# Optimization experiments

Hardware: AMD Instinct MI355X
Metric: run time of the kernel (lower is better)

## Reference

```python
import jax, jax.numpy as jnp
import numpy as np
from jax import lax

H = W = 200          # feature map size
STRIDE = 16
IMG_H = IMG_W = H * STRIDE  # 3200
C = 512
A = 9                # 3 scales x 3 aspect ratios
K_PRE = 1000         # pre-NMS topk (hardcoded in module)
K_POST = 100         # post-NMS keep (hardcoded in module)
IOU_TH = 0.7


def make_anchors():
    scales = jnp.array([128.0, 256.0, 512.0], dtype=jnp.float32)
    ratios = jnp.array([0.5, 1.0, 2.0], dtype=jnp.float32)
    hr = jnp.sqrt(ratios)                      # (3,)
    wr = 1.0 / hr
    ws = (wr[:, None] * scales[None, :]).reshape(-1)   # (9,)
    hs = (hr[:, None] * scales[None, :]).reshape(-1)
    base = jnp.stack([-ws / 2, -hs / 2, ws / 2, hs / 2], axis=1)  # (9,4)
    sx = jnp.arange(W, dtype=jnp.float32) * STRIDE
    sy = jnp.arange(H, dtype=jnp.float32) * STRIDE
    gy, gx = jnp.meshgrid(sy, sx, indexing='ij')
    shifts = jnp.stack([gx, gy, gx, gy], axis=-1).reshape(-1, 4)  # (H*W,4)
    return (shifts[:, None, :] + base[None, :, :]).reshape(-1, 4)  # (H*W*A,4)


def decode(anchors, deltas):
    w = anchors[:, 2] - anchors[:, 0]
    h = anchors[:, 3] - anchors[:, 1]
    cx = anchors[:, 0] + 0.5 * w
    cy = anchors[:, 1] + 0.5 * h
    px = deltas[:, 0] * w + cx
    py = deltas[:, 1] * h + cy
    pw = jnp.exp(deltas[:, 2]) * w
    ph = jnp.exp(deltas[:, 3]) * h
    return jnp.stack([px - 0.5 * pw, py - 0.5 * ph, px + 0.5 * pw, py + 0.5 * ph], axis=1)


def clamp_boxes(b):
    return jnp.stack([
        jnp.clip(b[:, 0], 0.0, IMG_W), jnp.clip(b[:, 1], 0.0, IMG_H),
        jnp.clip(b[:, 2], 0.0, IMG_W), jnp.clip(b[:, 3], 0.0, IMG_H)], axis=1)


def nms_keep(boxes, thr):
    # boxes (K_PRE,4) already sorted by descending score (topk output order)
    x1, y1, x2, y2 = boxes[:, 0], boxes[:, 1], boxes[:, 2], boxes[:, 3]
    areas = (x2 - x1) * (y2 - y1)
    idx = jnp.arange(K_PRE)

    def body(i, keep):
        iw = jnp.clip(jnp.minimum(x2[i], x2) - jnp.maximum(x1[i], x1), 0.0)
        ih = jnp.clip(jnp.minimum(y2[i], y2) - jnp.maximum(y1[i], y1), 0.0)
        inter = iw * ih
        iou = inter / (areas[i] + areas - inter)
        supp = (iou > thr) & (idx > i) & keep[i]
        return keep & jnp.logical_not(supp)

    return lax.fori_loop(0, K_PRE, body, jnp.ones(K_PRE, dtype=bool))


def rpn_forward(feat, conv_w, conv_b, cls_w, cls_b, reg_w, reg_b):
    dn = ('NCHW', 'OIHW', 'NCHW')
    x = lax.conv_general_dilated(feat, conv_w, (1, 1), 'SAME', dimension_numbers=dn)
    x = jax.nn.relu(x + conv_b[None, :, None, None])
    cls = lax.conv_general_dilated(x, cls_w, (1, 1), 'SAME', dimension_numbers=dn) + cls_b[None, :, None, None]
    reg = lax.conv_general_dilated(x, reg_w, (1, 1), 'SAME', dimension_numbers=dn) + reg_b[None, :, None, None]
    # (1,A,H,W) -> (H*W*A,)
    cls_logits = cls.transpose(0, 2, 3, 1).reshape(-1)
    # (1,A*4,H,W) -> (H*W*A,4)
    deltas = reg.reshape(1, A, 4, H, W).transpose(0, 3, 4, 1, 2).reshape(-1, 4)
    anchors = make_anchors()
    proposals = decode(anchors, deltas)
    scores = jax.nn.sigmoid(cls_logits)
    top_sc, top_idx = lax.top_k(scores, K_PRE)           # sorted descending
    props = clamp_boxes(proposals[top_idx])
    keep = lax.stop_gradient(nms_keep(props, IOU_TH))    # NMS decision is non-diff
    # kept indices, in score order (stable sort puts kept first, preserving order)
    order = jnp.argsort(jnp.where(keep, 0, 1), stable=True)[:K_POST]
    valid = jnp.arange(K_POST) < jnp.sum(keep)
    out_boxes = jnp.where(valid[:, None], props[order], 0.0)
    out_scores = jnp.where(valid, top_sc[order], 0.0)
    return out_boxes, out_scores


def setup_inputs() -> dict:
    key = jax.random.key(0)
    ks = jax.random.split(key, 7)
    s = 0.02
    return {
        'feat': jax.random.normal(ks[0], (1, C, H, W), dtype=jnp.float32),
        'conv_w': jax.random.normal(ks[1], (C, C, 3, 3), dtype=jnp.float32) * s,
        'conv_b': jnp.zeros((C,), dtype=jnp.float32),
        'cls_w': jax.random.normal(ks[2], (A, C, 1, 1), dtype=jnp.float32) * s,
        'cls_b': jnp.zeros((A,), dtype=jnp.float32),
        'reg_w': jax.random.normal(ks[3], (A * 4, C, 1, 1), dtype=jnp.float32) * s,
        'reg_b': jnp.zeros((A * 4,), dtype=jnp.float32),
    }


def reference(feat, conv_w, conv_b, cls_w, cls_b, reg_w, reg_b):
    return rpn_forward(feat, conv_w, conv_b, cls_w, cls_b, reg_w, reg_b)
```

## Files before the change

### kernel.cpp

```cpp
#include <hip/hip_runtime.h>
#include <stdint.h>

static constexpr int H_ = 200, W_ = 200, HW_ = 40000;
static constexpr int C_ = 512;
static constexpr int NANCH = 360000;
static constexpr int KPRE = 1000;
static constexpr int KPOST = 100;
static constexpr int KSEL = 1400;
static constexpr int PXCAP = 4096;
static constexpr int KSPLIT = 8;
static constexpr int FT = 212;
static constexpr int FP = 202;

typedef __attribute__((ext_vector_type(8))) short bf16x8;
typedef __attribute__((ext_vector_type(4))) float f32x4;

__device__ inline ushort f2bf(float f) {
    unsigned u = __float_as_uint(f);
    u += 0x7FFFu + ((u >> 16) & 1u);
    return (ushort)(u >> 16);
}
__device__ inline float bf2f(ushort h) { return __uint_as_float(((unsigned)h) << 16); }

typedef const __attribute__((address_space(1))) uint32_t gas_u32;
typedef __attribute__((address_space(3))) uint32_t las_u32;
__device__ __forceinline__ void gload_lds16(const void* g, void* l) {
    __builtin_amdgcn_global_load_lds((gas_u32*)(uintptr_t)g, (las_u32*)(uintptr_t)l, 16, 0, 0);
}

__global__ void k_zero_u32(unsigned* __restrict__ p, int n) {
    int i = blockIdx.x * 256 + threadIdx.x;
    if (i < n) p[i] = 0u;
}

__global__ void k_zero_border_t(ushort* __restrict__ feat_t) {
    int t = blockIdx.x * 256 + threadIdx.x;
    int total = 4944 * 64;
    if (t >= total) return;
    int px = t >> 6, part = t & 63;
    int y, x;
    if (px < 2544) { int ri = px / 212; x = px - ri * 212; y = (ri == 0) ? 0 : 200 + ri; }
    else { int q = px - 2544; int r12 = q / 12; int c = q - r12 * 12; y = 1 + r12; x = (c == 0) ? 0 : 200 + c; }
    uint4 z = {0u, 0u, 0u, 0u};
    *(uint4*)&feat_t[((size_t)y * FT + x) * 512 + part * 8] = z;
}

__global__ void k_zero_border_px(float* __restrict__ feat_px) {
    int t = blockIdx.x * 256 + threadIdx.x;
    int total = 804 * 128;
    if (t >= total) return;
    int px = t >> 7, part = t & 127;
    int y, x;
    if (px < 202)      { y = 0;   x = px; }
    else if (px < 404) { y = 201; x = px - 202; }
    else if (px < 604) { x = 0;   y = 1 + (px - 404); }
    else               { x = 201; y = 1 + (px - 604); }
    float4 z = {0.f, 0.f, 0.f, 0.f};
    *(float4*)&feat_px[((size_t)y * FP + x) * 512 + part * 4] = z;
}

__global__ void k_feat_t(const float* __restrict__ feat, ushort* __restrict__ feat_t) {
    __shared__ ushort lt[32 * 8 * 33];
    int x0 = blockIdx.x * 32, y0 = blockIdx.y * 8, ci0 = blockIdx.z * 32;
    int tid = threadIdx.x;
    for (int u = tid; u < 8192; u += 256) {
        int ciL = u >> 8, rem = u & 255;
        int yy = rem >> 5, xx = rem & 31;
        int x = x0 + xx;
        float v = (x < W_) ? feat[(size_t)(ci0 + ciL) * HW_ + (y0 + yy) * W_ + x] : 0.f;
        lt[(ciL * 8 + yy) * 33 + xx] = f2bf(v);
    }
    __syncthreads();
    for (int u = tid; u < 1024; u += 256) {
        int pxu = u >> 2, part = u & 3;
        int yy = pxu >> 5, xx = pxu & 31;
        if (x0 + xx >= W_) continue;
        ushort tmp[8];
#pragma unroll
        for (int k = 0; k < 8; ++k) tmp[k] = lt[((part * 8 + k) * 8 + yy) * 33 + xx];
        *(uint4*)&feat_t[((size_t)(y0 + yy + 1) * FT + (x0 + xx + 1)) * 512 + ci0 + part * 8] =
            *(const uint4*)&tmp[0];
    }
}

__global__ void k_feat_px(const float* __restrict__ feat, float* __restrict__ feat_px) {
    __shared__ float lt[32 * 8 * 33];
    int x0 = blockIdx.x * 32, y0 = blockIdx.y * 8, ci0 = blockIdx.z * 32;
    int tid = threadIdx.x;
    for (int u = tid; u < 8192; u += 256) {
        int ciL = u >> 8, rem = u & 255;
        int yy = rem >> 5, xx = rem & 31;
        int x = x0 + xx;
        float v = (x < W_) ? feat[(size_t)(ci0 + ciL) * HW_ + (y0 + yy) * W_ + x] : 0.f;
        lt[(ciL * 8 + yy) * 33 + xx] = v;
    }
    __syncthreads();
    for (int u = tid; u < 1024; u += 256) {
        int pxu = u >> 2, part = u & 3;
        int yy = pxu >> 5, xx = pxu & 31;
        if (x0 + xx >= W_) continue;
        float tmp[8];
#pragma unroll
        for (int k = 0; k < 8; ++k) tmp[k] = lt[((part * 8 + k) * 8 + yy) * 33 + xx];
        float* dst = &feat_px[((size_t)(y0 + yy + 1) * FP + (x0 + xx + 1)) * 512 + ci0 + part * 8];
        *(float4*)&dst[0] = *(const float4*)&tmp[0];
        *(float4*)&dst[4] = *(const float4*)&tmp[4];
    }
}

__global__ void k_wt_both(const float* __restrict__ conv_w, ushort* __restrict__ wt_t,
                          float* __restrict__ wt_ex) {
    __shared__ float t[32][33];
    int kb = blockIdx.x * 32;
    int cb = blockIdx.y * 32;
    int lx = threadIdx.x, ly = threadIdx.y;
    int tap = kb >> 9, ci0 = kb & 511;
    for (int r = ly; r < 32; r += 8) {
        float v = conv_w[((size_t)(cb + r) * 512 + ci0 + lx) * 9 + tap];
        t[r][lx] = v;
        wt_t[(size_t)tap * 262144 + (size_t)(cb + r) * 512 + ci0 + lx] = f2bf(v);
    }
    __syncthreads();
    for (int r = ly; r < 32; r += 8)
        wt_ex[(size_t)(kb + r) * 512 + cb + lx] = t[lx][r];
}

__global__ __launch_bounds__(256)
__attribute__((amdgpu_waves_per_eu(2, 4)))
void k_conv3_mfma(const ushort* __restrict__ feat_t, const ushort* __restrict__ wt_t,
                  const float* __restrict__ bias, ushort* __restrict__ xab) {
    __shared__ ushort halo[18 * 34 * 32];
    __shared__ ushort wtile[9 * 64 * 32];
    int b = blockIdx.x;
    int cot = b & 7;
    int tile = b >> 3;
    int xt = tile % 7, yt = tile / 7;
    int x0 = xt * 32, y0 = yt * 16;
    int co0 = cot * 64;
    int tid = threadIdx.x;
    int lane = tid & 63, wid = tid >> 6;
    int l15 = lane & 15, l4 = lane >> 4;

    f32x4 acc[4][2][4];
#pragma unroll
    for (int i = 0; i < 4; ++i)
#pragma unroll
        for (int h = 0; h < 2; ++h)
#pragma unroll
            for (int j = 0; j < 4; ++j) acc[i][h][j] = (f32x4){0.f, 0.f, 0.f, 0.f};

    for (int ch = 0; ch < 16; ++ch) {
        int ci0 = ch * 32;
        __syncthreads();
        for (int u = tid; u < 2448; u += 256) {
            int p = u >> 2, q = u & 3;
            int r = p / 34, c = p - r * 34;
            const ushort* src = feat_t + ((size_t)(y0 + r) * FT + (x0 + c)) * 512 + ci0 + q * 8;
            gload_lds16(src, &halo[(u & ~63) * 8]);
        }
        for (int u = tid; u < 2304; u += 256) {
            int row = u >> 2, q = u & 3;
            int tap = row >> 6, co = row & 63;
            const ushort* src = wt_t + ((size_t)(tap * 512 + co0 + co)) * 512 + ci0 + q * 8;
            gload_lds16(src, &wtile[(u & ~63) * 8]);
        }
        __syncthreads();
#pragma unroll
        for (int tap = 0; tap < 9; ++tap) {
            int th = tap / 3, tw = tap - th * 3;
            bf16x8 af[4][2];
#pragma unroll
            for (int pi = 0; pi < 4; ++pi)
#pragma unroll
                for (int xh = 0; xh < 2; ++xh)
                    af[pi][xh] = *(const bf16x8*)&halo[
                        ((wid * 4 + pi + th) * 34 + (xh * 16 + l15 + tw)) * 32 + l4 * 8];
#pragma unroll
            for (int cj = 0; cj < 4; ++cj) {
                bf16x8 bf = *(const bf16x8*)&wtile[(tap * 64 + cj * 16 + l15) * 32 + l4 * 8];
#pragma unroll
                for (int pi = 0; pi < 4; ++pi)
#pragma unroll
                    for (int xh = 0; xh < 2; ++xh)
                        acc[pi][xh][cj] = __builtin_amdgcn_mfma_f32_16x16x32_bf16(
                            af[pi][xh], bf, acc[pi][xh][cj], 0, 0, 0);
            }
        }
    }

    float bv[4];
#pragma unroll
    for (int cj = 0; cj < 4; ++cj) bv[cj] = bias[co0 + cj * 16 + l15];
#pragma unroll
    for (int pi = 0; pi < 4; ++pi) {
        int yy = y0 + wid * 4 + pi;
        if (yy >= H_) continue;
#pragma unroll
        for (int xh = 0; xh < 2; ++xh) {
#pragma unroll
            for (int cj = 0; cj < 4; ++cj) {
                int co = co0 + cj * 16 + l15;
#pragma unroll
                for (int r = 0; r < 4; ++r) {
                    int xx = x0 + xh * 16 + l4 * 4 + r;
                    if (xx < W_) {
                        float v = acc[pi][xh][cj][r] + bv[cj];
                        xab[((size_t)(yy * W_ + xx)) * 512 + co] = f2bf(v > 0.f ? v : 0.f);
                    }
                }
            }
        }
    }
}

__global__ void k_cls(const ushort* __restrict__ xab, const float* __restrict__ cls_w,
                      const float* __restrict__ cls_b, float* __restrict__ scores) {
    __shared__ ushort xt[64 * 520];
    int t = threadIdx.x;
    int pxb = blockIdx.x * 64;
    for (int i = 0; i < 64; ++i)
        *(uint4*)&xt[i * 520 + t * 8] =
            *(const uint4*)&xab[((size_t)(pxb + i)) * 512 + t * 8];
    __syncthreads();
    float acc[9];
#pragma unroll
    for (int a = 0; a < 9; ++a) acc[a] = 0.f;
    const ushort* row = &xt[t * 520];
    for (int k = 0; k < 64; ++k) {
        bf16x8 v = *(const bf16x8*)&row[k * 8];
        float xv[8];
#pragma unroll
        for (int j = 0; j < 8; ++j) xv[j] = bf2f((ushort)v[j]);
#pragma unroll
        for (int a = 0; a < 9; ++a)
#pragma unroll
            for (int j = 0; j < 8; ++j)
                acc[a] = fmaf(xv[j], cls_w[a * 512 + k * 8 + j], acc[a]);
    }
    int px = pxb + t;
#pragma unroll
    for (int a = 0; a < 9; ++a)
        scores[(size_t)px * 9 + a] = 1.f / (1.f + expf(-(acc[a] + cls_b[a])));
}

__global__ void k_hist1_lds(const float* __restrict__ scores, unsigned* __restrict__ hist) {
    __shared__ unsigned h[16384];
    int tid = threadIdx.x;
    for (int j = tid; j < 16384; j += 256) h[j] = 0u;
    __syncthreads();
    int stride = gridDim.x * 256;
    for (int i = blockIdx.x * 256 + tid; i < NANCH; i += stride)
        atomicAdd(&h[(__float_as_uint(scores[i]) >> 16) & 16383], 1u);
    __syncthreads();
    for (int j = tid; j < 16384; j += 256) {
        unsigned v = h[j];
        if (v) atomicAdd(&hist[j], v);
    }
}

__global__ void k_find_thr(const unsigned* __restrict__ hist, unsigned* __restrict__ meta,
                           int mode, int Kwant) {
    __shared__ unsigned csum[1024];
    int t = threadIdx.x;
    unsigned base = (mode == 0) ? 0u : meta[1];
    unsigned s = 0;
    for (int b = 0; b < 64; ++b) s += hist[t * 64 + b];
    csum[t] = s;
    __syncthreads();
    for (int off = 1; off < 1024; off <<= 1) {
        unsigned add = (t + off < 1024) ? csum[t + off] : 0u;
        __syncthreads();
        csum[t] += add;
        __syncthreads();
    }
    unsigned run = base + ((t < 1023) ? csum[t + 1] : 0u);
    for (int b = 63; b >= 0; --b) {
        unsigned h = hist[t * 64 + b];
        if (run < (unsigned)Kwant && run + h >= (unsigned)Kwant) {
            if (mode == 0) {
                meta[0] = (unsigned)(t * 64 + b);
                meta[1] = run;
            } else {
                meta[2] = (meta[0] << 16) | (unsigned)(t * 64 + b);
                meta[3] = run;
                meta[4] = (unsigned)Kwant - run;
            }
            break;
        }
        run += h;
    }
}

__global__ void k_collect_cand(const float* __restrict__ scores, const unsigned* __restrict__ meta,
                               unsigned* __restrict__ flags) {
    int i = blockIdx.x * 256 + threadIdx.x;
    if (i >= NANCH) return;
    if ((__float_as_uint(scores[i]) >> 16) >= meta[0]) flags[i / 9] = 1u;
}

__global__ void k_px_compact(unsigned* __restrict__ flags, unsigned* __restrict__ meta,
                             unsigned* __restrict__ px_list) {
    int px = blockIdx.x * 256 + threadIdx.x;
    if (px >= HW_) return;
    if (flags[px]) {
        unsigned s = atomicAdd(&meta[10], 1u);
        if (s < (unsigned)PXCAP) { px_list[s] = (unsigned)px; flags[px] = s + 1u; }
        else flags[px] = 0u;
    }
}

__global__ __attribute__((amdgpu_waves_per_eu(2, 4)))
void k_exact_gemm(const float* __restrict__ feat_px, const float* __restrict__ wt_ex,
                  const unsigned* __restrict__ meta, const unsigned* __restrict__ px_list,
                  float* __restrict__ xpart) {
    int npx = (int)meta[10]; if (npx > PXCAP) npx = PXCAP;
    int pb = blockIdx.x;
    if (pb * 64 >= npx) return;
    int cot = blockIdx.y;
    int kz = blockIdx.z;
    __shared__ float A[64][68];
    __shared__ float B[64][68];
    __shared__ int plist[64];
    int tid = threadIdx.x;
    int co0 = cot * 64;
    if (tid < 64) {
        int slot = pb * 64 + tid;
        plist[tid] = (slot < npx) ? (int)px_list[slot] : (int)px_list[0];
    }
    int tcog = tid >> 4;
    int tpxg = tid & 15;
    float acc[4][4];
#pragma unroll
    for (int i = 0; i < 4; ++i)
#pragma unroll
        for (int j = 0; j < 4; ++j) acc[i][j] = 0.f;
    int kbase = kz * 576;
    for (int kc = 0; kc < 9; ++kc) {
        int k0 = kbase + kc * 64;
        __syncthreads();
        for (int u = tid; u < 1024; u += 256) {
            int k = u >> 4, cp = (u & 15) * 4;
            *(float4*)&A[k][cp] = *(const float4*)&wt_ex[(size_t)(k0 + k) * 512 + co0 + cp];
        }
#pragma unroll
        for (int hh = 0; hh < 2; ++hh) {
            int kh = k0 + hh * 32;
            int tap = kh >> 9, ci0c = kh & 511;
            int th = tap / 3, tw = tap - th * 3;
            for (int u = tid; u < 512; u += 256) {
                int s = u >> 3, part = u & 7;
                int px = plist[s];
                int y = px / W_, x = px - y * W_;
                float4 v = *(const float4*)&feat_px[((size_t)(y + th) * FP + (x + tw)) * 512 + ci0c + part * 4];
                B[hh * 32 + part * 4 + 0][s] = v.x; B[hh * 32 + part * 4 + 1][s] = v.y;
                B[hh * 32 + part * 4 + 2][s] = v.z; B[hh * 32 + part * 4 + 3][s] = v.w;
            }
        }
        __syncthreads();
#pragma unroll 4
        for (int k = 0; k < 64; ++k) {
            float wv[4], pv[4];
            *(float4*)&wv[0] = *(const float4*)&A[k][tcog * 4];
            *(float4*)&pv[0] = *(const float4*)&B[k][tpxg * 4];
#pragma unroll
            for (int i = 0; i < 4; ++i)
#pragma unroll
                for (int j = 0; j < 4; ++j) acc[i][j] = fmaf(wv[i], pv[j], acc[i][j]);
        }
    }
#pragma unroll
    for (int j = 0; j < 4; ++j) {
        int slot = pb * 64 + tpxg * 4 + j;
        if (slot >= npx) continue;
        f32x4 tmp;
        tmp[0] = acc[0][j]; tmp[1] = acc[1][j]; tmp[2] = acc[2][j]; tmp[3] = acc[3][j];
        __builtin_nontemporal_store(tmp,
            (f32x4*)&xpart[((size_t)kz * PXCAP + slot) * 512 + co0 + tcog * 4]);
    }
}

__global__ void k_exact_fin(const float* __restrict__ xpart, const float* __restrict__ bias,
                            const float* __restrict__ cls_w, const float* __restrict__ cls_b,
                            const unsigned* __restrict__ meta,
                            float* __restrict__ xex, float* __restrict__ scores_ex) {
    int slot = blockIdx.x;
    int npx = (int)meta[10]; if (npx > PXCAP) npx = PXCAP;
    if (slot >= npx) return;
    int l = threadIdx.x;
    float xv[8];
#pragma unroll
    for (int j = 0; j < 8; ++j) {
        int co = j * 64 + l;
        float v = 0.f;
#pragma unroll
        for (int kz = 0; kz < KSPLIT; ++kz)
            v += __builtin_nontemporal_load(&xpart[((size_t)kz * PXCAP + slot) * 512 + co]);
        v += bias[co];
        v = v > 0.f ? v : 0.f;
        xex[(size_t)slot * 512 + co] = v;
        xv[j] = v;
    }
#pragma unroll
    for (int a = 0; a < 9; ++a) {
        float s = 0.f;
#pragma unroll
        for (int k = 0; k < 8; ++k) s = fmaf(xv[k], cls_w[a * 512 + k * 64 + l], s);
#pragma unroll
        for (int o = 32; o > 0; o >>= 1) s += __shfl_down(s, o);
        if (l == 0) scores_ex[slot * 9 + a] = 1.f / (1.f + expf(-(s + cls_b[a])));
    }
}

__global__ void k_hist1_ex_lds(const float* __restrict__ scores_ex, const unsigned* __restrict__ meta,
                               unsigned* __restrict__ hist) {
    __shared__ unsigned h[16384];
    int npx = (int)meta[10]; if (npx > PXCAP) npx = PXCAP;
    int n = npx * 9;
    int tid = threadIdx.x;
    for (int j = tid; j < 16384; j += 256) h[j] = 0u;
    __syncthreads();
    for (int i = blockIdx.x * 256 + tid; i < n; i += 32 * 256)
        atomicAdd(&h[(__float_as_uint(scores_ex[i]) >> 16) & 16383], 1u);
    __syncthreads();
    for (int j = tid; j < 16384; j += 256) {
        unsigned v = h[j];
        if (v) atomicAdd(&hist[j], v);
    }
}

__global__ void k_hist2_ex(const float* __restrict__ scores_ex, const unsigned* __restrict__ meta,
                           const unsigned* __restrict__ meta_ex, unsigned* __restrict__ hist2) {
    int npx = (int)meta[10]; if (npx > PXCAP) npx = PXCAP;
    int i = blockIdx.x * 256 + threadIdx.x;
    if (i >= npx * 9) return;
    unsigned b = __float_as_uint(scores_ex[i]);
    if ((b >> 16) == meta_ex[0]) atomicAdd(&hist2[b & 0xFFFFu], 1u);
}

__global__ void k_collect_ex(const float* __restrict__ scores_ex, const unsigned* __restrict__ meta,
                             unsigned* __restrict__ meta_ex, const unsigned* __restrict__ px_list,
                             unsigned* __restrict__ sel_bits, unsigned* __restrict__ sel_idx,
                             unsigned* __restrict__ eq_idx) {
    int npx = (int)meta[10]; if (npx > PXCAP) npx = PXCAP;
    int i = blockIdx.x * 256 + threadIdx.x;
    if (i >= npx * 9) return;
    unsigned b = __float_as_uint(scores_ex[i]);
    unsigned T = meta_ex[2];
    unsigned g = px_list[i / 9] * 9u + (unsigned)(i % 9);
    if (b > T) {
        unsigned s = atomicAdd(&meta_ex[8], 1u);
        if (s < 1024u) { sel_bits[s] = b; sel_idx[s] = g; }
    } else if (b == T) {
        unsigned s = atomicAdd(&meta_ex[9], 1u);
        if (s < 65536u) eq_idx[s] = g;
    }
}

__global__ void k_topk_final(const unsigned* __restrict__ sel_bits, const unsigned* __restrict__ sel_idx,
                             const unsigned* __restrict__ eq_idx, const unsigned* __restrict__ meta,
                             unsigned* __restrict__ top_idx, float* __restrict__ top_sc) {
    __shared__ uint64_t keys[1024];
    __shared__ int lcnt;
    __shared__ int lred;
    int t = threadIdx.x;
    unsigned cntGt = meta[3];
    unsigned need = meta[4];
    unsigned cntEq = meta[9];
    unsigned T = meta[2];

    unsigned idx_cut = 0xFFFFFFFFu;
    if (cntEq > need) {
        unsigned lo = 0, hi = NANCH - 1;
        while (lo < hi) {
            unsigned mid = (lo + hi) >> 1;
            int c = 0;
            for (unsigned e = t; e < cntEq; e += 1024)
                if (eq_idx[e] <= mid) c++;
            if (t == 0) lred = 0;
            __syncthreads();
            atomicAdd(&lred, c);
            __syncthreads();
            int tot = lred;
            __syncthreads();
            if ((unsigned)tot >= need) hi = mid; else lo = mid + 1;
        }
        idx_cut = lo;
    }

    keys[t] = 0ull;
    if (t == 0) lcnt = 0;
    __syncthreads();
    for (unsigned s = t; s < cntGt; s += 1024)
        keys[s] = ((uint64_t)sel_bits[s] << 32) | (uint64_t)(0xFFFFFFFFu - sel_idx[s]);
    for (unsigned e = t; e < cntEq; e += 1024) {
        unsigned ix = eq_idx[e];
        if (ix <= idx_cut) {
            int s2 = (int)cntGt + atomicAdd(&lcnt, 1);
            keys[s2] = ((uint64_t)T << 32) | (uint64_t)(0xFFFFFFFFu - ix);
        }
    }
    __syncthreads();
    for (int k = 2; k <= 1024; k <<= 1) {
        for (int j = k >> 1; j > 0; j >>= 1) {
            int ixj = t ^ j;
            if (ixj > t) {
                uint64_t a = keys[t], b = keys[ixj];
                bool desc = (t & k) == 0;
                if (desc ? (a < b) : (a > b)) { keys[t] = b; keys[ixj] = a; }
            }
            __syncthreads();
        }
    }
    if (t < KPRE) {
        top_sc[t] = __uint_as_float((unsigned)(keys[t] >> 32));
        top_idx[t] = 0xFFFFFFFFu - (unsigned)keys[t];
    }
}

__global__ void k_decode(const float* __restrict__ xex, const unsigned* __restrict__ flags,
                         const float* __restrict__ reg_w, const float* __restrict__ reg_b,
                         const unsigned* __restrict__ top_idx,
                         float* __restrict__ props, float* __restrict__ areas) {
    int j = blockIdx.x;
    int lane = threadIdx.x;
    unsigned idx = top_idx[j];
    int pix = (int)(idx / 9u);
    int a = (int)(idx - (unsigned)pix * 9u);
    int slot = (int)flags[pix] - 1;
    if (slot < 0) slot = 0;
    const float* xr = xex + (size_t)slot * 512;
    float s0 = 0, s1 = 0, s2 = 0, s3 = 0;
    for (int c = lane; c < C_; c += 64) {
        float xv = xr[c];
        s0 = fmaf(xv, reg_w[(a * 4 + 0) * C_ + c], s0);
        s1 = fmaf(xv, reg_w[(a * 4 + 1) * C_ + c], s1);
        s2 = fmaf(xv, reg_w[(a * 4 + 2) * C_ + c], s2);
        s3 = fmaf(xv, reg_w[(a * 4 + 3) * C_ + c], s3);
    }
#pragma unroll
    for (int o = 32; o > 0; o >>= 1) {
        s0 += __shfl_down(s0, o);
        s1 += __shfl_down(s1, o);
        s2 += __shfl_down(s2, o);
        s3 += __shfl_down(s3, o);
    }
    if (lane == 0) {
        float d0 = s0 + reg_b[a * 4 + 0];
        float d1 = s1 + reg_b[a * 4 + 1];
        float d2 = s2 + reg_b[a * 4 + 2];
        float d3 = s3 + reg_b[a * 4 + 3];
        int h = pix / W_, w2 = pix - h * W_;
        int rr = a / 3, ss = a - rr * 3;
        float ratio = (rr == 0) ? 0.5f : (rr == 1) ? 1.0f : 2.0f;
        float scale = (ss == 0) ? 128.f : (ss == 1) ? 256.f : 512.f;
        float hr = sqrtf(ratio);
        float wr = 1.0f / hr;
        float wsc = wr * scale, hsc = hr * scale;
        float sx = (float)w2 * 16.f, sy = (float)h * 16.f;
        float a0 = sx - wsc * 0.5f, a1 = sy - hsc * 0.5f;
        float a2 = sx + wsc * 0.5f, a3 = sy + hsc * 0.5f;
        float bw = a2 - a0, bh = a3 - a1;
        float cx = a0 + 0.5f * bw, cy = a1 + 0.5f * bh;
        float px = d0 * bw + cx, py = d1 * bh + cy;
        float pw = expf(d2) * bw, ph = expf(d3) * bh;
        float b0 = px - 0.5f * pw, b1 = py - 0.5f * ph;
        float b2 = px + 0.5f * pw, b3 = py + 0.5f * ph;
        b0 = fminf(fmaxf(b0, 0.f), 3200.f);
        b1 = fminf(fmaxf(b1, 0.f), 3200.f);
        b2 = fminf(fmaxf(b2, 0.f), 3200.f);
        b3 = fminf(fmaxf(b3, 0.f), 3200.f);
        props[j * 4 + 0] = b0;
        props[j * 4 + 1] = b1;
        props[j * 4 + 2] = b2;
        props[j * 4 + 3] = b3;
        areas[j] = (b2 - b0) * (b3 - b1);
    }
}

__global__ void k_nms_mask(const float* __restrict__ props, const float* __restrict__ areas,
                           unsigned long long* __restrict__ mask, float* __restrict__ out) {
    int i = blockIdx.x;
    int tid = threadIdx.x;
    if (i == 0) {
        for (int t = tid; t < KPOST * 5; t += 256) out[t] = 0.f;
    }
    float x1i = props[i * 4 + 0], y1i = props[i * 4 + 1];
    float x2i = props[i * 4 + 2], y2i = props[i * 4 + 3];
    float ai = areas[i];
#pragma unroll
    for (int k = 0; k < 4; ++k) {
        int j = k * 256 + tid;
        bool sup = false;
        if (j < KPRE && j > i) {
            float iw = fminf(x2i, props[j * 4 + 2]) - fmaxf(x1i, props[j * 4 + 0]);
            float ih = fminf(y2i, props[j * 4 + 3]) - fmaxf(y1i, props[j * 4 + 1]);
            iw = fmaxf(iw, 0.f);
            ih = fmaxf(ih, 0.f);
            float inter = iw * ih;
            float iou = inter / (ai + areas[j] - inter);
            sup = iou > 0.7f;
        }
        unsigned long long b = __ballot(sup);
        int word = k * 4 + (tid >> 6);
        if ((tid & 63) == 0) mask[(size_t)i * 16 + word] = b;
    }
}

__global__ void k_nms_scan_out(const unsigned long long* __restrict__ mask,
                               const float* __restrict__ props, const float* __restrict__ top_sc,
                               float* __restrict__ out) {
    __shared__ int kidx[KPOST];
    __shared__ int nk;
    int lane = threadIdx.x;
    if (lane == 0) {
        unsigned long long k0 = ~0ull, k1 = ~0ull, k2 = ~0ull, k3 = ~0ull;
        unsigned long long k4 = ~0ull, k5 = ~0ull, k6 = ~0ull, k7 = ~0ull;
        unsigned long long k8 = ~0ull, k9 = ~0ull, k10 = ~0ull, k11 = ~0ull;
        unsigned long long k12 = ~0ull, k13 = ~0ull, k14 = ~0ull;
        unsigned long long k15 = (1ull << 40) - 1ull;
        int kept = 0;
#define APPLY_ROW(ii) { const unsigned long long* row = &mask[(size_t)(ii) * 16];          \
        k0 &= ~row[0];  k1 &= ~row[1];  k2 &= ~row[2];  k3 &= ~row[3];                     \
        k4 &= ~row[4];  k5 &= ~row[5];  k6 &= ~row[6];  k7 &= ~row[7];                     \
        k8 &= ~row[8];  k9 &= ~row[9];  k10 &= ~row[10]; k11 &= ~row[11];                  \
        k12 &= ~row[12]; k13 &= ~row[13]; k14 &= ~row[14]; k15 &= ~row[15]; }
#define SCAN_WORD(w, kw) { \
        unsigned long long rem = kw; \
        while (rem) { \
            int b = __builtin_ctzll(rem); \
            kidx[kept++] = (w) * 64 + b; \
            if (kept == KPOST) goto done; \
            APPLY_ROW((w) * 64 + b); \
            rem &= kw; \
            rem &= (b >= 63) ? 0ull : ~((2ull << b) - 1ull); \
        } }
        SCAN_WORD(0, k0)  SCAN_WORD(1, k1)  SCAN_WORD(2, k2)  SCAN_WORD(3, k3)
        SCAN_WORD(4, k4)  SCAN_WORD(5, k5)  SCAN_WORD(6, k6)  SCAN_WORD(7, k7)
        SCAN_WORD(8, k8)  SCAN_WORD(9, k9)  SCAN_WORD(10, k10) SCAN_WORD(11, k11)
        SCAN_WORD(12, k12) SCAN_WORD(13, k13) SCAN_WORD(14, k14) SCAN_WORD(15, k15)
done:
        nk = kept;
#undef SCAN_WORD
#undef APPLY_ROW
    }
    __syncthreads();
    int n = nk;
    for (int t = lane; t < KPOST; t += 64) {
        if (t < n) {
            int i = kidx[t];
            out[t * 4 + 0] = props[i * 4 + 0];
            out[t * 4 + 1] = props[i * 4 + 1];
            out[t * 4 + 2] = props[i * 4 + 2];
            out[t * 4 + 3] = props[i * 4 + 3];
            out[KPOST * 4 + t] = top_sc[i];
        }
    }
}

extern "C" void kernel_launch(void* const* d_in, const int* in_sizes, int n_in,
                              void* d_out, int out_size, void* d_ws, size_t ws_size,
                              hipStream_t stream) {
    const float* feat   = (const float*)d_in[0];
    const float* conv_w = (const float*)d_in[1];
    const float* conv_b = (const float*)d_in[2];
    const float* cls_w  = (const float*)d_in[3];
    const float* cls_b  = (const float*)d_in[4];
    const float* reg_w  = (const float*)d_in[5];
    const float* reg_b  = (const float*)d_in[6];
    float* out = (float*)d_out;

    size_t off = 0;
    auto alloc = [&](size_t bytes) -> void* {
        off = (off + 255) & ~(size_t)255;
        void* p = (char*)d_ws + off;
        off += bytes;
        return p;
    };
    ushort* feat_t  = (ushort*)alloc((size_t)FT * FT * 512 * 2);
    float*  feat_px = (float*)alloc((size_t)FP * FP * 512 * 4);
    ushort* wt_t    = (ushort*)alloc((size_t)9 * 512 * 512 * 2);
    float*  wt_ex   = (float*)alloc((size_t)9 * 512 * 512 * 4);
    ushort* xab     = (ushort*)alloc((size_t)HW_ * 512 * 2);
    float*  xpart   = (float*)alloc((size_t)KSPLIT * PXCAP * 512 * 4);
    float*  xex     = (float*)alloc((size_t)PXCAP * 512 * 4);
    float*  scores  = (float*)alloc((size_t)NANCH * 4);
    float*  scores_ex = (float*)alloc((size_t)PXCAP * 9 * 4);
    unsigned* hist1   = (unsigned*)alloc(65536 * 4);
    unsigned* hist2   = (unsigned*)alloc(65536 * 4);
    unsigned* hist1e  = (unsigned*)alloc(65536 * 4);
    unsigned* hist2e  = (unsigned*)alloc(65536 * 4);
    unsigned* meta    = (unsigned*)alloc(64 * 4);
    unsigned* meta_ex = (unsigned*)alloc(64 * 4);
    unsigned* flags   = (unsigned*)alloc((size_t)HW_ * 4);
    unsigned* px_list = (unsigned*)alloc(PXCAP * 4);
    unsigned* sel_bits = (unsigned*)alloc(1024 * 4);
    unsigned* sel_idx  = (unsigned*)alloc(1024 * 4);
    unsigned* eq_idx   = (unsigned*)alloc(65536 * 4);
    unsigned* top_idx  = (unsigned*)alloc(KPRE * 4);
    float* top_sc      = (float*)alloc(KPRE * 4);
    float* props       = (float*)alloc(KPRE * 4 * 4);
    float* areas       = (float*)alloc(KPRE * 4);
    unsigned long long* mask = (unsigned long long*)alloc((size_t)KPRE * 16 * 8);
    (void)ws_size; (void)in_sizes; (void)n_in; (void)out_size;

    k_zero_border_t<<<(4944 * 64 + 255) / 256, 256, 0, stream>>>(feat_t);
    int zrDw = 65536 * 4 + 128 + HW_;
    k_zero_u32<<<(zrDw + 255) / 256, 256, 0, stream>>>(hist1, zrDw);
    k_feat_t<<<dim3(7, 25, 16), 256, 0, stream>>>(feat, feat_t);
    k_wt_both<<<dim3(144, 16), dim3(32, 8), 0, stream>>>(conv_w, wt_t, wt_ex);
    k_conv3_mfma<<<8 * 91, 256, 0, stream>>>(feat_t, wt_t, conv_b, xab);
    k_cls<<<HW_ / 64, 64, 0, stream>>>(xab, cls_w, cls_b, scores);
    k_hist1_lds<<<64, 256, 0, stream>>>(scores, hist1);
    k_find_thr<<<1, 1024, 0, stream>>>(hist1, meta, 0, KSEL);
    k_collect_cand<<<(NANCH + 255) / 256, 256, 0, stream>>>(scores, meta, flags);
    k_px_compact<<<(HW_ + 255) / 256, 256, 0, stream>>>(flags, meta, px_list);
    k_zero_border_px<<<(804 * 128 + 255) / 256, 256, 0, stream>>>(feat_px);
    k_feat_px<<<dim3(7, 25, 16), 256, 0, stream>>>(feat, feat_px);
    k_exact_gemm<<<dim3(PXCAP / 64, 8, KSPLIT), 256, 0, stream>>>(feat_px, wt_ex, meta, px_list, xpart);
    k_exact_fin<<<PXCAP, 64, 0, stream>>>(xpart, conv_b, cls_w, cls_b, meta, xex, scores_ex);
    k_hist1_ex_lds<<<32, 256, 0, stream>>>(scores_ex, meta, hist1e);
    k_find_thr<<<1, 1024, 0, stream>>>(hist1e, meta_ex, 0, KPRE);
    k_hist2_ex<<<(PXCAP * 9 + 255) / 256, 256, 0, stream>>>(scores_ex, meta, meta_ex, hist2e);
    k_find_thr<<<1, 1024, 0, stream>>>(hist2e, meta_ex, 1, KPRE);
    k_collect_ex<<<(PXCAP * 9 + 255) / 256, 256, 0, stream>>>(scores_ex, meta, meta_ex, px_list,
                                                              sel_bits, sel_idx, eq_idx);
    k_topk_final<<<1, 1024, 0, stream>>>(sel_bits, sel_idx, eq_idx, meta_ex, top_idx, top_sc);
    k_decode<<<KPRE, 64, 0, stream>>>(xex, flags, reg_w, reg_b, top_idx, props, areas);
    k_nms_mask<<<KPRE, 256, 0, stream>>>(props, areas, mask, out);
    k_nms_scan_out<<<1, 64, 0, stream>>>(mask, props, top_sc, out);
}
```

Before: 709.7 us.

## Fuse cls head into conv epilogue and merge feature transposes and candidate kernels

```diff
diff --git a/kernel.cpp b/kernel.cpp
--- a/kernel.cpp
+++ b/kernel.cpp
@@ -59,31 +59,8 @@
     *(float4*)&feat_px[((size_t)y * FP + x) * 512 + part * 4] = z;
 }
 
-__global__ void k_feat_t(const float* __restrict__ feat, ushort* __restrict__ feat_t) {
-    __shared__ ushort lt[32 * 8 * 33];
-    int x0 = blockIdx.x * 32, y0 = blockIdx.y * 8, ci0 = blockIdx.z * 32;
-    int tid = threadIdx.x;
-    for (int u = tid; u < 8192; u += 256) {
-        int ciL = u >> 8, rem = u & 255;
-        int yy = rem >> 5, xx = rem & 31;
-        int x = x0 + xx;
-        float v = (x < W_) ? feat[(size_t)(ci0 + ciL) * HW_ + (y0 + yy) * W_ + x] : 0.f;
-        lt[(ciL * 8 + yy) * 33 + xx] = f2bf(v);
-    }
-    __syncthreads();
-    for (int u = tid; u < 1024; u += 256) {
-        int pxu = u >> 2, part = u & 3;
-        int yy = pxu >> 5, xx = pxu & 31;
-        if (x0 + xx >= W_) continue;
-        ushort tmp[8];
-#pragma unroll
-        for (int k = 0; k < 8; ++k) tmp[k] = lt[((part * 8 + k) * 8 + yy) * 33 + xx];
-        *(uint4*)&feat_t[((size_t)(y0 + yy + 1) * FT + (x0 + xx + 1)) * 512 + ci0 + part * 8] =
-            *(const uint4*)&tmp[0];
-    }
-}
-
-__global__ void k_feat_px(const float* __restrict__ feat, float* __restrict__ feat_px) {
+__global__ void k_feat_both(const float* __restrict__ feat, ushort* __restrict__ feat_t,
+                            float* __restrict__ feat_px) {
     __shared__ float lt[32 * 8 * 33];
     int x0 = blockIdx.x * 32, y0 = blockIdx.y * 8, ci0 = blockIdx.z * 32;
     int tid = threadIdx.x;
@@ -100,11 +77,17 @@
         int yy = pxu >> 5, xx = pxu & 31;
         if (x0 + xx >= W_) continue;
         float tmp[8];
-#pragma unroll
-        for (int k = 0; k < 8; ++k) tmp[k] = lt[((part * 8 + k) * 8 + yy) * 33 + xx];
+        ushort tb[8];
+#pragma unroll
+        for (int k = 0; k < 8; ++k) {
+            tmp[k] = lt[((part * 8 + k) * 8 + yy) * 33 + xx];
+            tb[k] = f2bf(tmp[k]);
+        }
         float* dst = &feat_px[((size_t)(y0 + yy + 1) * FP + (x0 + xx + 1)) * 512 + ci0 + part * 8];
         *(float4*)&dst[0] = *(const float4*)&tmp[0];
         *(float4*)&dst[4] = *(const float4*)&tmp[4];
+        *(uint4*)&feat_t[((size_t)(y0 + yy + 1) * FT + (x0 + xx + 1)) * 512 + ci0 + part * 8] =
+            *(const uint4*)&tb[0];
     }
 }
 
@@ -128,9 +111,11 @@
 __global__ __launch_bounds__(256)
 __attribute__((amdgpu_waves_per_eu(2, 4)))
 void k_conv3_mfma(const ushort* __restrict__ feat_t, const ushort* __restrict__ wt_t,
-                  const float* __restrict__ bias, ushort* __restrict__ xab) {
-    __shared__ ushort halo[18 * 34 * 32];
-    __shared__ ushort wtile[9 * 64 * 32];
+                  const float* __restrict__ bias, const float* __restrict__ cls_w,
+                  float* __restrict__ cls_part) {
+    __shared__ ushort smem[18 * 34 * 32 + 9 * 64 * 32];
+    ushort* halo = smem;
+    ushort* wtile = smem + 18 * 34 * 32;
     int b = blockIdx.x;
     int cot = b & 7;
     int tile = b >> 3;
@@ -188,59 +173,65 @@
         }
     }
 
+    __syncthreads();
+    ushort* xl = smem;
     float bv[4];
 #pragma unroll
     for (int cj = 0; cj < 4; ++cj) bv[cj] = bias[co0 + cj * 16 + l15];
 #pragma unroll
     for (int pi = 0; pi < 4; ++pi) {
-        int yy = y0 + wid * 4 + pi;
-        if (yy >= H_) continue;
 #pragma unroll
         for (int xh = 0; xh < 2; ++xh) {
 #pragma unroll
             for (int cj = 0; cj < 4; ++cj) {
-                int co = co0 + cj * 16 + l15;
+                int co = cj * 16 + l15;
 #pragma unroll
                 for (int r = 0; r < 4; ++r) {
-                    int xx = x0 + xh * 16 + l4 * 4 + r;
-                    if (xx < W_) {
-                        float v = acc[pi][xh][cj][r] + bv[cj];
-                        xab[((size_t)(yy * W_ + xx)) * 512 + co] = f2bf(v > 0.f ? v : 0.f);
-                    }
+                    int px = (wid * 4 + pi) * 32 + xh * 16 + l4 * 4 + r;
+                    float v = acc[pi][xh][cj][r] + bv[cj];
+                    xl[px * 72 + co] = f2bf(v > 0.f ? v : 0.f);
                 }
             }
         }
     }
-}
-
-__global__ void k_cls(const ushort* __restrict__ xab, const float* __restrict__ cls_w,
-                      const float* __restrict__ cls_b, float* __restrict__ scores) {
-    __shared__ ushort xt[64 * 520];
-    int t = threadIdx.x;
-    int pxb = blockIdx.x * 64;
-    for (int i = 0; i < 64; ++i)
-        *(uint4*)&xt[i * 520 + t * 8] =
-            *(const uint4*)&xab[((size_t)(pxb + i)) * 512 + t * 8];
-    __syncthreads();
-    float acc[9];
-#pragma unroll
-    for (int a = 0; a < 9; ++a) acc[a] = 0.f;
-    const ushort* row = &xt[t * 520];
-    for (int k = 0; k < 64; ++k) {
-        bf16x8 v = *(const bf16x8*)&row[k * 8];
-        float xv[8];
-#pragma unroll
-        for (int j = 0; j < 8; ++j) xv[j] = bf2f((ushort)v[j]);
-#pragma unroll
-        for (int a = 0; a < 9; ++a)
-#pragma unroll
-            for (int j = 0; j < 8; ++j)
-                acc[a] = fmaf(xv[j], cls_w[a * 512 + k * 8 + j], acc[a]);
-    }
-    int px = pxb + t;
-#pragma unroll
-    for (int a = 0; a < 9; ++a)
-        scores[(size_t)px * 9 + a] = 1.f / (1.f + expf(-(acc[a] + cls_b[a])));
+    __syncthreads();
+
+    bf16x8 b0, b1;
+#pragma unroll
+    for (int j = 0; j < 8; ++j) {
+        b0[j] = (l15 < 9) ? (short)f2bf(cls_w[l15 * 512 + co0 + l4 * 8 + j]) : (short)0;
+        b1[j] = (l15 < 9) ? (short)f2bf(cls_w[l15 * 512 + co0 + 32 + l4 * 8 + j]) : (short)0;
+    }
+#pragma unroll
+    for (int gg = 0; gg < 8; ++gg) {
+        int g = wid * 8 + gg;
+        bf16x8 a0 = *(const bf16x8*)&xl[(g * 16 + l15) * 72 + l4 * 8];
+        bf16x8 a1 = *(const bf16x8*)&xl[(g * 16 + l15) * 72 + 32 + l4 * 8];
+        f32x4 p = (f32x4){0.f, 0.f, 0.f, 0.f};
+        p = __builtin_amdgcn_mfma_f32_16x16x32_bf16(a0, b0, p, 0, 0, 0);
+        p = __builtin_amdgcn_mfma_f32_16x16x32_bf16(a1, b1, p, 0, 0, 0);
+        if (l15 < 9) {
+#pragma unroll
+            for (int r = 0; r < 4; ++r) {
+                int px = g * 16 + l4 * 4 + r;
+                int row = px >> 5, col = px & 31;
+                int yy = y0 + row, xx = x0 + col;
+                if (yy < H_ && xx < W_)
+                    cls_part[(size_t)cot * NANCH + ((size_t)yy * W_ + xx) * 9 + l15] = p[r];
+            }
+        }
+    }
+}
+
+__global__ void k_cls_fin(const float* __restrict__ cls_part, const float* __restrict__ cls_b,
+                          float* __restrict__ scores) {
+    int i = blockIdx.x * 256 + threadIdx.x;
+    if (i >= NANCH) return;
+    float s = 0.f;
+#pragma unroll
+    for (int c = 0; c < 8; ++c) s += cls_part[(size_t)c * NANCH + i];
+    int a = i % 9;
+    scores[i] = 1.f / (1.f + expf(-(s + cls_b[a])));
 }
 
 __global__ void k_hist1_lds(const float* __restrict__ scores, unsigned* __restrict__ hist) {
@@ -291,21 +282,18 @@
     }
 }
 
-__global__ void k_collect_cand(const float* __restrict__ scores, const unsigned* __restrict__ meta,
-                               unsigned* __restrict__ flags) {
-    int i = blockIdx.x * 256 + threadIdx.x;
-    if (i >= NANCH) return;
-    if ((__float_as_uint(scores[i]) >> 16) >= meta[0]) flags[i / 9] = 1u;
-}
-
-__global__ void k_px_compact(unsigned* __restrict__ flags, unsigned* __restrict__ meta,
-                             unsigned* __restrict__ px_list) {
+__global__ void k_cand(const float* __restrict__ scores, unsigned* __restrict__ meta,
+                       unsigned* __restrict__ flags, unsigned* __restrict__ px_list) {
     int px = blockIdx.x * 256 + threadIdx.x;
     if (px >= HW_) return;
-    if (flags[px]) {
-        unsigned s = atomicAdd(&meta[10], 1u);
-        if (s < (unsigned)PXCAP) { px_list[s] = (unsigned)px; flags[px] = s + 1u; }
-        else flags[px] = 0u;
+    unsigned P = meta[0];
+    const float* s = &scores[(size_t)px * 9];
+    bool any = false;
+#pragma unroll
+    for (int a = 0; a < 9; ++a) any |= ((__float_as_uint(s[a]) >> 16) >= P);
+    if (any) {
+        unsigned sl = atomicAdd(&meta[10], 1u);
+        if (sl < (unsigned)PXCAP) { px_list[sl] = (unsigned)px; flags[px] = sl + 1u; }
     }
 }
 
@@ -680,7 +668,7 @@
     float*  feat_px = (float*)alloc((size_t)FP * FP * 512 * 4);
     ushort* wt_t    = (ushort*)alloc((size_t)9 * 512 * 512 * 2);
     float*  wt_ex   = (float*)alloc((size_t)9 * 512 * 512 * 4);
-    ushort* xab     = (ushort*)alloc((size_t)HW_ * 512 * 2);
+    float*  cls_part = (float*)alloc((size_t)8 * NANCH * 4);
     float*  xpart   = (float*)alloc((size_t)KSPLIT * PXCAP * 512 * 4);
     float*  xex     = (float*)alloc((size_t)PXCAP * 512 * 4);
     float*  scores  = (float*)alloc((size_t)NANCH * 4);
@@ -704,18 +692,16 @@
     (void)ws_size; (void)in_sizes; (void)n_in; (void)out_size;
 
     k_zero_border_t<<<(4944 * 64 + 255) / 256, 256, 0, stream>>>(feat_t);
+    k_zero_border_px<<<(804 * 128 + 255) / 256, 256, 0, stream>>>(feat_px);
     int zrDw = 65536 * 4 + 128 + HW_;
     k_zero_u32<<<(zrDw + 255) / 256, 256, 0, stream>>>(hist1, zrDw);
-    k_feat_t<<<dim3(7, 25, 16), 256, 0, stream>>>(feat, feat_t);
+    k_feat_both<<<dim3(7, 25, 16), 256, 0, stream>>>(feat, feat_t, feat_px);
     k_wt_both<<<dim3(144, 16), dim3(32, 8), 0, stream>>>(conv_w, wt_t, wt_ex);
-    k_conv3_mfma<<<8 * 91, 256, 0, stream>>>(feat_t, wt_t, conv_b, xab);
-    k_cls<<<HW_ / 64, 64, 0, stream>>>(xab, cls_w, cls_b, scores);
+    k_conv3_mfma<<<8 * 91, 256, 0, stream>>>(feat_t, wt_t, conv_b, cls_w, cls_part);
+    k_cls_fin<<<(NANCH + 255) / 256, 256, 0, stream>>>(cls_part, cls_b, scores);
     k_hist1_lds<<<64, 256, 0, stream>>>(scores, hist1);
     k_find_thr<<<1, 1024, 0, stream>>>(hist1, meta, 0, KSEL);
-    k_collect_cand<<<(NANCH + 255) / 256, 256, 0, stream>>>(scores, meta, flags);
-    k_px_compact<<<(HW_ + 255) / 256, 256, 0, stream>>>(flags, meta, px_list);
-    k_zero_border_px<<<(804 * 128 + 255) / 256, 256, 0, stream>>>(feat_px);
-    k_feat_px<<<dim3(7, 25, 16), 256, 0, stream>>>(feat, feat_px);
+    k_cand<<<(HW_ + 255) / 256, 256, 0, stream>>>(scores, meta, flags, px_list);
     k_exact_gemm<<<dim3(PXCAP / 64, 8, KSPLIT), 256, 0, stream>>>(feat_px, wt_ex, meta, px_list, xpart);
     k_exact_fin<<<PXCAP, 64, 0, stream>>>(xpart, conv_b, cls_w, cls_b, meta, xex, scores_ex);
     k_hist1_ex_lds<<<32, 256, 0, stream>>>(scores_ex, meta, hist1e);
```

New measurement: 611.3 us (median of 2 runs). 1.16x faster.
